# Kernel optimization log

Hardware: AMD Instinct MI355X
Metric: run time of the kernel (lower is better)

## Reference

```python
import jax, jax.numpy as jnp
import numpy as np

TOP_K = 8
SCALE = 2.5  # moe_router_scaling_factor
EPS = 1e-20


def setup_inputs() -> dict:
    key = jax.random.key(0)
    k1, k2 = jax.random.split(key)
    B, S, H, E = 4, 4096, 4096, 64
    hidden_states = jax.random.normal(k1, (B, S, H), dtype=jnp.float32)
    gate_weight = jax.random.normal(k2, (E, H), dtype=jnp.float32) * 0.02
    router_bias = jnp.zeros((E,), dtype=jnp.float32)
    return {"hidden_states": hidden_states, "gate_weight": gate_weight, "router_bias": router_bias}


def reference(hidden_states, gate_weight, router_bias):
    B, S, H = hidden_states.shape
    x = hidden_states.reshape(-1, H).astype(jnp.float32)  # [T, H]
    # need_fp32_gate: fp32 matmul against gate weight transpose -> [T, E]
    logits = jnp.einsum('th,eh->te', x, gate_weight.astype(jnp.float32))
    gate_prob = jax.nn.sigmoid(logits)
    biased = gate_prob + router_bias[None, :]
    # topk on bias-shifted probs; weights gathered from UNbiased probs
    _, indices = jax.lax.top_k(biased, TOP_K)                       # [T, K]
    topk_prob = jnp.take_along_axis(gate_prob, indices, axis=1)     # [T, K]
    weights = topk_prob / (jnp.sum(topk_prob, axis=-1, keepdims=True) + EPS)
    weights = weights * SCALE
    return weights, indices
```

## Files before the change

kernel.cpp:

```cpp
#include <hip/hip_runtime.h>
#include <cmath>


typedef float f32x4 __attribute__((ext_vector_type(4)));
typedef short s16x8 __attribute__((ext_vector_type(8)));
typedef unsigned int u32;
typedef u32 u32x4 __attribute__((ext_vector_type(4)));

#define E_DIM 64
#define KC 32
#define CH_BYTES 12288
#define NPART 4
#define HI_OFF (2u << 20)

union V16 { u32x4 u; s16x8 s; };

__device__ __forceinline__ unsigned short f2bf(float f) {
  unsigned u = __float_as_uint(f);
  u += 0x7fffu + ((u >> 16) & 1u);
  return (unsigned short)(u >> 16);
}
__device__ __forceinline__ float bf2f(unsigned short s) {
  return __uint_as_float(((unsigned)s) << 16);
}

__global__ __launch_bounds__(256) void split_w(
    const float* __restrict__ w, unsigned char* __restrict__ w3, int Hdim)
{
  const int kpr = Hdim >> 4;
  const int g = blockIdx.x * 256 + threadIdx.x;
  const int e = g / kpr;
  const int k0 = (g - e * kpr) * 16;
  if (e >= E_DIM) return;

  const float* src = w + (size_t)e * Hdim + k0;
  float f[16];
#pragma unroll
  for (int i = 0; i < 4; ++i) {
    float4 v = *(const float4*)(src + i * 4);
    f[i*4+0] = v.x; f[i*4+1] = v.y; f[i*4+2] = v.z; f[i*4+3] = v.w;
  }
  unsigned short hs[16], ms[16], ls[16];
#pragma unroll
  for (int i = 0; i < 16; ++i) {
    unsigned short h = f2bf(f[i]);
    float r1 = f[i] - bf2f(h);
    unsigned short m = f2bf(r1);
    float r2 = r1 - bf2f(m);
    hs[i] = h; ms[i] = m; ls[i] = f2bf(r2);
  }
  const int c  = k0 >> 5;
  const int n  = e >> 4;
  const int la = (e & 15) + (((k0 & 31) >> 3) << 4);
  unsigned char* base = w3 + (size_t)c * CH_BYTES + n * 1024;

#define STORE_SPLIT(arr, s)                                              \
  do {                                                                   \
    s16x8 pa, pb;                                                        \
    _Pragma("unroll")                                                    \
    for (int j = 0; j < 8; ++j) { pa[j] = (short)arr[j]; pb[j] = (short)arr[8+j]; } \
    *(s16x8*)(base + (s)*4096 + la * 16)        = pa;                    \
    *(s16x8*)(base + (s)*4096 + (la + 16) * 16) = pb;                    \
  } while (0)

  STORE_SPLIT(hs, 0);
  STORE_SPLIT(ms, 1);
  STORE_SPLIT(ls, 2);
#undef STORE_SPLIT
}

__global__ __launch_bounds__(256, 4) void router_mfma(
    const float* __restrict__ x, const unsigned char* __restrict__ w3,
    const float* __restrict__ bias, float* __restrict__ outw,
    float* __restrict__ outi, float2* __restrict__ pp,
    int T, int Hdim)
{
  __shared__ __align__(16) unsigned char lds[3 * CH_BYTES];

  const int tid  = threadIdx.x;
  const int wid  = tid >> 6;
  const int lane = tid & 63;
  const int lc   = lane & 15;
  const int lq   = lane >> 4;
  const int by   = blockIdx.y;
  const int nch  = Hdim / KC / gridDim.y;
  const int t0   = blockIdx.x * 64;

  const float* xp = x + (size_t)(t0 + wid * 16 + lc) * Hdim
                      + (size_t)by * nch * KC + lq * 8;
  const unsigned char* w3p = w3 + (size_t)by * nch * CH_BYTES;

  f32x4 acc[4], sum_[4], comp[4];
#pragma unroll
  for (int n = 0; n < 4; ++n) {
    acc[n] = (f32x4){0,0,0,0};
    sum_[n] = (f32x4){0,0,0,0};
    comp[n] = (f32x4){0,0,0,0};
  }

#define SB()     __builtin_amdgcn_sched_barrier(0)
#define WAITV5() asm volatile("s_waitcnt vmcnt(5)" ::: "memory")
#define WAITV0() asm volatile("s_waitcnt vmcnt(0)" ::: "memory")
#define BAR()    __builtin_amdgcn_s_barrier()

#define STAGE(c, so)                                                         \
  do {                                                                       \
    const unsigned char* gs = w3p + (size_t)(c) * CH_BYTES + tid * 16;       \
    unsigned char* ld_ = &lds[0] + (so) + tid * 16;                          \
    _Pragma("unroll")                                                        \
    for (int i = 0; i < 3; ++i)                                              \
      __builtin_amdgcn_global_load_lds(                                      \
          (const __attribute__((address_space(1))) unsigned int*)(gs + i*4096), \
          (__attribute__((address_space(3))) unsigned int*)(ld_ + i*4096),   \
          16, 0, 0);                                                         \
  } while (0)

#define LOADX(c, X)                                                          \
  do {                                                                       \
    X[0] = *(const float4*)(xp + (size_t)(c) * KC);                          \
    X[1] = *(const float4*)(xp + (size_t)(c) * KC + 4);                      \
  } while (0)

#define SPLIT_PAIR(f0, f1, i, AHU, AMU, ALU)                                 \
  do {                                                                       \
    u32 u0_ = __float_as_uint(f0), u1_ = __float_as_uint(f1);                \
    u32 v0_ = u0_ + 0x8000u, v1_ = u1_ + 0x8000u;                            \
    AHU[i] = __builtin_amdgcn_perm(v1_, v0_, 0x07060302u);                   \
    float r0_ = (f0) - __uint_as_float(v0_ & 0xffff0000u);                   \
    float r1_ = (f1) - __uint_as_float(v1_ & 0xffff0000u);                   \
    u32 w0_ = __float_as_uint(r0_) + 0x8000u;                                \
    u32 w1_ = __float_as_uint(r1_) + 0x8000u;                                \
    AMU[i] = __builtin_amdgcn_perm(w1_, w0_, 0x07060302u);                   \
    float s0_ = r0_ - __uint_as_float(w0_ & 0xffff0000u);                    \
    float s1_ = r1_ - __uint_as_float(w1_ & 0xffff0000u);                    \
    u32 y0_ = __float_as_uint(s0_) + 0x8000u;                                \
    u32 y1_ = __float_as_uint(s1_) + 0x8000u;                                \
    ALU[i] = __builtin_amdgcn_perm(y1_, y0_, 0x07060302u);                   \
  } while (0)

#define CONVERT(X)                                                           \
  do {                                                                       \
    V16 ah_, am_, al_;                                                       \
    SPLIT_PAIR(X[0].x, X[0].y, 0, ah_.u, am_.u, al_.u);                      \
    SPLIT_PAIR(X[0].z, X[0].w, 1, ah_.u, am_.u, al_.u);                      \
    SPLIT_PAIR(X[1].x, X[1].y, 2, ah_.u, am_.u, al_.u);                      \
    SPLIT_PAIR(X[1].z, X[1].w, 3, ah_.u, am_.u, al_.u);                      \
    Aah = ah_.s; Aam = am_.s; Aal = al_.s;                                   \
  } while (0)

#define MFMA_ALL(ro)                                                         \
  do {                                                                       \
    const unsigned char* B_ = &lds[0] + (ro) + lane * 16;                    \
    __builtin_amdgcn_s_setprio(1);                                           \
    _Pragma("unroll")                                                        \
    for (int g = 0; g < 2; ++g) {                                            \
      s16x8 bh0 = *(const s16x8*)(B_ + 0*4096 + (2*g)*1024);                 \
      s16x8 bh1 = *(const s16x8*)(B_ + 0*4096 + (2*g+1)*1024);               \
      s16x8 bm0 = *(const s16x8*)(B_ + 1*4096 + (2*g)*1024);                 \
      s16x8 bm1 = *(const s16x8*)(B_ + 1*4096 + (2*g+1)*1024);               \
      s16x8 bl0 = *(const s16x8*)(B_ + 2*4096 + (2*g)*1024);                 \
      s16x8 bl1 = *(const s16x8*)(B_ + 2*4096 + (2*g+1)*1024);               \
      acc[2*g]   = __builtin_amdgcn_mfma_f32_16x16x32_bf16(Aah, bh0, acc[2*g],   0,0,0); \
      acc[2*g+1] = __builtin_amdgcn_mfma_f32_16x16x32_bf16(Aah, bh1, acc[2*g+1], 0,0,0); \
      acc[2*g]   = __builtin_amdgcn_mfma_f32_16x16x32_bf16(Aah, bm0, acc[2*g],   0,0,0); \
      acc[2*g+1] = __builtin_amdgcn_mfma_f32_16x16x32_bf16(Aah, bm1, acc[2*g+1], 0,0,0); \
      acc[2*g]   = __builtin_amdgcn_mfma_f32_16x16x32_bf16(Aam, bh0, acc[2*g],   0,0,0); \
      acc[2*g+1] = __builtin_amdgcn_mfma_f32_16x16x32_bf16(Aam, bh1, acc[2*g+1], 0,0,0); \
      acc[2*g]   = __builtin_amdgcn_mfma_f32_16x16x32_bf16(Aah, bl0, acc[2*g],   0,0,0); \
      acc[2*g+1] = __builtin_amdgcn_mfma_f32_16x16x32_bf16(Aah, bl1, acc[2*g+1], 0,0,0); \
      acc[2*g]   = __builtin_amdgcn_mfma_f32_16x16x32_bf16(Aam, bm0, acc[2*g],   0,0,0); \
      acc[2*g+1] = __builtin_amdgcn_mfma_f32_16x16x32_bf16(Aam, bm1, acc[2*g+1], 0,0,0); \
      acc[2*g]   = __builtin_amdgcn_mfma_f32_16x16x32_bf16(Aal, bh0, acc[2*g],   0,0,0); \
      acc[2*g+1] = __builtin_amdgcn_mfma_f32_16x16x32_bf16(Aal, bh1, acc[2*g+1], 0,0,0); \
    }                                                                        \
    __builtin_amdgcn_s_setprio(0);                                           \
  } while (0)

#define FOLD()                                                               \
  do {                                                                       \
    _Pragma("unroll")                                                        \
    for (int n = 0; n < 4; ++n)                                              \
      _Pragma("unroll")                                                      \
      for (int r = 0; r < 4; ++r) {                                          \
        float a_ = acc[n][r];                                                \
        float s_ = sum_[n][r];                                               \
        float t_ = s_ + a_;                                                  \
        float z_ = t_ - s_;                                                  \
        comp[n][r] += (s_ - (t_ - z_)) + (a_ - z_);                          \
        sum_[n][r] = t_;                                                     \
        acc[n][r] = 0.f;                                                     \
      }                                                                      \
  } while (0)

#define ITER(c, ro, so, XBUF)                                                \
  do {                                                                       \
    STAGE((c) + 2, so);                                                      \
    CONVERT(XBUF);                                                           \
    LOADX((c) + 2, XBUF);                                                    \
    SB();                                                                    \
    MFMA_ALL(ro);                                                            \
    WAITV5();                                                                \
    BAR();                                                                   \
  } while (0)

  float4 XA[2], XB[2];
  s16x8 Aah, Aam, Aal;

  int ro0 = 0, ro1 = CH_BYTES, ro2 = 2 * CH_BYTES;

  STAGE(0, ro0);
  STAGE(1, ro1);
  LOADX(0, XA);
  LOADX(1, XB);

#pragma unroll 1
  for (int c = 0; c < nch - 4; c += 4) {
    ITER(c + 0, ro0, ro2, XA);
    ITER(c + 1, ro1, ro0, XB);
    ITER(c + 2, ro2, ro1, XA);
    ITER(c + 3, ro0, ro2, XB);
    FOLD();
    int t_ = ro0; ro0 = ro1; ro1 = ro2; ro2 = t_;
  }
  ITER(nch - 4, ro0, ro2, XA);
  ITER(nch - 3, ro1, ro0, XB);
  {
    CONVERT(XA);
    SB();
    MFMA_ALL(ro2);
    WAITV0();
    BAR();
    CONVERT(XB);
    SB();
    MFMA_ALL(ro0);
    FOLD();
  }

  if (gridDim.y != 1) {
#pragma unroll
    for (int n = 0; n < 4; ++n)
#pragma unroll
      for (int r = 0; r < 4; ++r) {
        const int tok = t0 + wid * 16 + lq * 4 + r;
        const size_t o = ((size_t)tok * NPART + by) * E_DIM + n * 16 + lc;
        pp[o] = make_float2(sum_[n][r], comp[n][r]);
      }
    return;
  }

  float bias_v[4];
#pragma unroll
  for (int n = 0; n < 4; ++n) bias_v[n] = bias[n * 16 + lc];

  float pr[4][4], bi[4][4];
#pragma unroll
  for (int n = 0; n < 4; ++n)
#pragma unroll
    for (int r = 0; r < 4; ++r) {
      float logit = sum_[n][r] + comp[n][r];
      float p = 1.0f / (1.0f + expf(-logit));
      pr[n][r] = p;
      bi[n][r] = p + bias_v[n];
    }
#pragma unroll
  for (int r = 0; r < 4; ++r) {
    float v0 = bi[0][r], v1 = bi[1][r], v2 = bi[2][r], v3 = bi[3][r];
    float p0 = pr[0][r], p1 = pr[1][r], p2 = pr[2][r], p3 = pr[3][r];
    float sum = 0.f, selp = 0.f;
    int seli = 0;
#pragma unroll
    for (int k = 0; k < 8; ++k) {
      float bv = v0; int bn = 0; float bp = p0;
      if (v1 > bv) { bv = v1; bn = 1; bp = p1; }
      if (v2 > bv) { bv = v2; bn = 2; bp = p2; }
      if (v3 > bv) { bv = v3; bn = 3; bp = p3; }
      int be = bn * 16 + lc;
#pragma unroll
      for (int off = 8; off >= 1; off >>= 1) {
        float ov = __shfl_xor(bv, off);
        float op = __shfl_xor(bp, off);
        int   oe = __shfl_xor(be, off);
        if (ov > bv || (ov == bv && oe < be)) { bv = ov; bp = op; be = oe; }
      }
      sum += bp;
      if (lc == k) { selp = bp; seli = be; }
      if (lc == (be & 15)) {
        int gsel = be >> 4;
        if      (gsel == 0) v0 = -1e30f;
        else if (gsel == 1) v1 = -1e30f;
        else if (gsel == 2) v2 = -1e30f;
        else                v3 = -1e30f;
      }
    }
    if (lc < 8) {
      const int tok = t0 + wid * 16 + lq * 4 + r;
      outw[(size_t)tok * 8 + lc] = selp * 2.5f / (sum + 1e-20f);
      outi[(size_t)tok * 8 + lc] = (float)seli;
    }
  }
}

__global__ __launch_bounds__(256) void router_topk(
    const float2* __restrict__ pp, const float* __restrict__ bias,
    float* __restrict__ outw, float* __restrict__ outi, int T)
{
  const int lane = threadIdx.x & 63;
  const int t = blockIdx.x * 4 + (threadIdx.x >> 6);
  if (t >= T) return;

  float s = 0.f, c = 0.f, losum = 0.f;
#pragma unroll
  for (int p = 0; p < NPART; ++p) {
    const float2 v = pp[((size_t)t * NPART + p) * E_DIM + lane];
    float a = v.x;
    float tt = s + a;
    float z = tt - s;
    c += (s - (tt - z)) + (a - z);
    s = tt;
    losum += v.y;
  }
  const float logit = s + (c + losum);

  const float prob = 1.0f / (1.0f + expf(-logit));
  float v = prob + bias[lane];

  float sum = 0.f, selw = 0.f;
  int seli = 0;
#pragma unroll
  for (int k = 0; k < 8; ++k) {
    float rv = v;
    int   ri = lane;
#pragma unroll
    for (int off = 32; off > 0; off >>= 1) {
      float ov = __shfl_xor(rv, off);
      int   oi = __shfl_xor(ri, off);
      if (ov > rv || (ov == rv && oi < ri)) { rv = ov; ri = oi; }
    }
    float pwin = __shfl(prob, ri);
    sum += pwin;
    if (lane == k)  { selw = pwin; seli = ri; }
    if (lane == ri) v = -INFINITY;
  }

  if (lane < 8) {
    float scale = 2.5f / (sum + 1e-20f);
    outw[(size_t)t * 8 + lane] = selw * scale;
    outi[(size_t)t * 8 + lane] = (float)seli;
  }
}

extern "C" void kernel_launch(void* const* d_in, const int* in_sizes, int n_in,
                              void* d_out, int out_size, void* d_ws, size_t ws_size,
                              hipStream_t stream) {
  const float* x    = (const float*)d_in[0];
  const float* w    = (const float*)d_in[1];
  const float* bias = (const float*)d_in[2];

  const int E    = in_sizes[2];
  const int Hdim = in_sizes[1] / E;
  const int T    = in_sizes[0] / Hdim;

  unsigned char* ws = (unsigned char*)d_ws;
  unsigned char* w3 = ws;
  float2* pp = (float2*)(ws + HI_OFF);

  const size_t need = (size_t)HI_OFF + (size_t)NPART * T * E_DIM * sizeof(float2);
  const int nparts = (ws_size >= need) ? NPART : 1;

  const int nElemGroups = E * Hdim / 16;
  split_w<<<(nElemGroups + 255) / 256, 256, 0, stream>>>(w, w3, Hdim);

  float* outw = (float*)d_out;
  float* outi = outw + (size_t)T * 8;

  dim3 gridG(T / 64, nparts);
  router_mfma<<<gridG, 256, 0, stream>>>(x, w3, bias, outw, outi, pp, T, Hdim);

  if (nparts != 1) {
    router_topk<<<(T + 3) / 4, 256, 0, stream>>>(pp, bias, outw, outi, T);
  }
}
```

Measured before the change: 109.9 us.

## Double-buffer weight LDS, split K eight ways, pack partials as single float

Shrinks the weight LDS ring from three stages to two, prefetching one chunk ahead instead of two, and raises the occupancy hint from 4 to 5 blocks per CU. The K dimension is split into 8 partitions instead of 4, doubling the grid. Each partition now writes one float (sum plus compensation) rather than a float2, and the top-k kernel drops its separate low-part sum. The MFMA loop is restructured to iterate per expert tile. The aim is more parallelism and occupancy, at the cost of a shallower prefetch that may expose load latency.

After: 138.9 us. +26.4%, slower.

```diff
diff --git a/kernel.cpp b/kernel.cpp
--- a/kernel.cpp
+++ b/kernel.cpp
@@ -10,7 +10,7 @@
 #define E_DIM 64
 #define KC 32
 #define CH_BYTES 12288
-#define NPART 4
+#define NPART 8
 #define HI_OFF (2u << 20)
 
 union V16 { u32x4 u; s16x8 s; };
@@ -69,13 +69,13 @@
 #undef STORE_SPLIT
 }
 
-__global__ __launch_bounds__(256, 4) void router_mfma(
+__global__ __launch_bounds__(256, 5) void router_mfma(
     const float* __restrict__ x, const unsigned char* __restrict__ w3,
     const float* __restrict__ bias, float* __restrict__ outw,
-    float* __restrict__ outi, float2* __restrict__ pp,
+    float* __restrict__ outi, float* __restrict__ pp,
     int T, int Hdim)
 {
-  __shared__ __align__(16) unsigned char lds[3 * CH_BYTES];
+  __shared__ __align__(16) unsigned char lds[2][CH_BYTES];
 
   const int tid  = threadIdx.x;
   const int wid  = tid >> 6;
@@ -99,14 +99,14 @@
   }
 
 #define SB()     __builtin_amdgcn_sched_barrier(0)
-#define WAITV5() asm volatile("s_waitcnt vmcnt(5)" ::: "memory")
+#define WAITV2() asm volatile("s_waitcnt vmcnt(2)" ::: "memory")
 #define WAITV0() asm volatile("s_waitcnt vmcnt(0)" ::: "memory")
 #define BAR()    __builtin_amdgcn_s_barrier()
 
-#define STAGE(c, so)                                                         \
+#define STAGE(c, b)                                                          \
   do {                                                                       \
     const unsigned char* gs = w3p + (size_t)(c) * CH_BYTES + tid * 16;       \
-    unsigned char* ld_ = &lds[0] + (so) + tid * 16;                          \
+    unsigned char* ld_ = &lds[b][0] + tid * 16;                              \
     _Pragma("unroll")                                                        \
     for (int i = 0; i < 3; ++i)                                              \
       __builtin_amdgcn_global_load_lds(                                      \
@@ -148,30 +148,21 @@
     Aah = ah_.s; Aam = am_.s; Aal = al_.s;                                   \
   } while (0)
 
-#define MFMA_ALL(ro)                                                         \
-  do {                                                                       \
-    const unsigned char* B_ = &lds[0] + (ro) + lane * 16;                    \
+#define MFMA_ALL(b)                                                          \
+  do {                                                                       \
+    const unsigned char* B_ = &lds[b][0] + lane * 16;                        \
     __builtin_amdgcn_s_setprio(1);                                           \
     _Pragma("unroll")                                                        \
-    for (int g = 0; g < 2; ++g) {                                            \
-      s16x8 bh0 = *(const s16x8*)(B_ + 0*4096 + (2*g)*1024);                 \
-      s16x8 bh1 = *(const s16x8*)(B_ + 0*4096 + (2*g+1)*1024);               \
-      s16x8 bm0 = *(const s16x8*)(B_ + 1*4096 + (2*g)*1024);                 \
-      s16x8 bm1 = *(const s16x8*)(B_ + 1*4096 + (2*g+1)*1024);               \
-      s16x8 bl0 = *(const s16x8*)(B_ + 2*4096 + (2*g)*1024);                 \
-      s16x8 bl1 = *(const s16x8*)(B_ + 2*4096 + (2*g+1)*1024);               \
-      acc[2*g]   = __builtin_amdgcn_mfma_f32_16x16x32_bf16(Aah, bh0, acc[2*g],   0,0,0); \
-      acc[2*g+1] = __builtin_amdgcn_mfma_f32_16x16x32_bf16(Aah, bh1, acc[2*g+1], 0,0,0); \
-      acc[2*g]   = __builtin_amdgcn_mfma_f32_16x16x32_bf16(Aah, bm0, acc[2*g],   0,0,0); \
-      acc[2*g+1] = __builtin_amdgcn_mfma_f32_16x16x32_bf16(Aah, bm1, acc[2*g+1], 0,0,0); \
-      acc[2*g]   = __builtin_amdgcn_mfma_f32_16x16x32_bf16(Aam, bh0, acc[2*g],   0,0,0); \
-      acc[2*g+1] = __builtin_amdgcn_mfma_f32_16x16x32_bf16(Aam, bh1, acc[2*g+1], 0,0,0); \
-      acc[2*g]   = __builtin_amdgcn_mfma_f32_16x16x32_bf16(Aah, bl0, acc[2*g],   0,0,0); \
-      acc[2*g+1] = __builtin_amdgcn_mfma_f32_16x16x32_bf16(Aah, bl1, acc[2*g+1], 0,0,0); \
-      acc[2*g]   = __builtin_amdgcn_mfma_f32_16x16x32_bf16(Aam, bm0, acc[2*g],   0,0,0); \
-      acc[2*g+1] = __builtin_amdgcn_mfma_f32_16x16x32_bf16(Aam, bm1, acc[2*g+1], 0,0,0); \
-      acc[2*g]   = __builtin_amdgcn_mfma_f32_16x16x32_bf16(Aal, bh0, acc[2*g],   0,0,0); \
-      acc[2*g+1] = __builtin_amdgcn_mfma_f32_16x16x32_bf16(Aal, bh1, acc[2*g+1], 0,0,0); \
+    for (int n = 0; n < 4; ++n) {                                            \
+      s16x8 bh = *(const s16x8*)(B_ + 0*4096 + n*1024);                      \
+      s16x8 bm = *(const s16x8*)(B_ + 1*4096 + n*1024);                      \
+      s16x8 bl = *(const s16x8*)(B_ + 2*4096 + n*1024);                      \
+      acc[n] = __builtin_amdgcn_mfma_f32_16x16x32_bf16(Aah, bh, acc[n], 0,0,0); \
+      acc[n] = __builtin_amdgcn_mfma_f32_16x16x32_bf16(Aah, bm, acc[n], 0,0,0); \
+      acc[n] = __builtin_amdgcn_mfma_f32_16x16x32_bf16(Aam, bh, acc[n], 0,0,0); \
+      acc[n] = __builtin_amdgcn_mfma_f32_16x16x32_bf16(Aah, bl, acc[n], 0,0,0); \
+      acc[n] = __builtin_amdgcn_mfma_f32_16x16x32_bf16(Aam, bm, acc[n], 0,0,0); \
+      acc[n] = __builtin_amdgcn_mfma_f32_16x16x32_bf16(Aal, bh, acc[n], 0,0,0); \
     }                                                                        \
     __builtin_amdgcn_s_setprio(0);                                           \
   } while (0)
@@ -192,47 +183,49 @@
       }                                                                      \
   } while (0)
 
-#define ITER(c, ro, so, XBUF)                                                \
-  do {                                                                       \
-    STAGE((c) + 2, so);                                                      \
+#define ITER(c, XBUF)                                                        \
+  do {                                                                       \
     CONVERT(XBUF);                                                           \
+    STAGE((c) + 1, ((c) + 1) & 1);                                           \
     LOADX((c) + 2, XBUF);                                                    \
     SB();                                                                    \
-    MFMA_ALL(ro);                                                            \
-    WAITV5();                                                                \
+    MFMA_ALL((c) & 1);                                                       \
+    WAITV2();                                                                \
     BAR();                                                                   \
+    SB();                                                                    \
   } while (0)
 
   float4 XA[2], XB[2];
   s16x8 Aah, Aam, Aal;
 
-  int ro0 = 0, ro1 = CH_BYTES, ro2 = 2 * CH_BYTES;
-
-  STAGE(0, ro0);
-  STAGE(1, ro1);
+  STAGE(0, 0);
   LOADX(0, XA);
   LOADX(1, XB);
+  asm volatile("s_waitcnt vmcnt(4)" ::: "memory");
+  BAR();
+  SB();
 
 #pragma unroll 1
   for (int c = 0; c < nch - 4; c += 4) {
-    ITER(c + 0, ro0, ro2, XA);
-    ITER(c + 1, ro1, ro0, XB);
-    ITER(c + 2, ro2, ro1, XA);
-    ITER(c + 3, ro0, ro2, XB);
+    ITER(c + 0, XA);
+    ITER(c + 1, XB);
+    ITER(c + 2, XA);
+    ITER(c + 3, XB);
     FOLD();
-    int t_ = ro0; ro0 = ro1; ro1 = ro2; ro2 = t_;
-  }
-  ITER(nch - 4, ro0, ro2, XA);
-  ITER(nch - 3, ro1, ro0, XB);
+  }
+  ITER(nch - 4, XA);
+  ITER(nch - 3, XB);
   {
     CONVERT(XA);
+    STAGE(nch - 1, 1);
     SB();
-    MFMA_ALL(ro2);
+    MFMA_ALL(0);
     WAITV0();
     BAR();
+    SB();
     CONVERT(XB);
     SB();
-    MFMA_ALL(ro0);
+    MFMA_ALL(1);
     FOLD();
   }
 
@@ -243,7 +236,7 @@
       for (int r = 0; r < 4; ++r) {
         const int tok = t0 + wid * 16 + lq * 4 + r;
         const size_t o = ((size_t)tok * NPART + by) * E_DIM + n * 16 + lc;
-        pp[o] = make_float2(sum_[n][r], comp[n][r]);
+        pp[o] = sum_[n][r] + comp[n][r];
       }
     return;
   }
@@ -301,25 +294,23 @@
 }
 
 __global__ __launch_bounds__(256) void router_topk(
-    const float2* __restrict__ pp, const float* __restrict__ bias,
+    const float* __restrict__ pp, const float* __restrict__ bias,
     float* __restrict__ outw, float* __restrict__ outi, int T)
 {
   const int lane = threadIdx.x & 63;
   const int t = blockIdx.x * 4 + (threadIdx.x >> 6);
   if (t >= T) return;
 
-  float s = 0.f, c = 0.f, losum = 0.f;
+  float s = 0.f, c = 0.f;
 #pragma unroll
   for (int p = 0; p < NPART; ++p) {
-    const float2 v = pp[((size_t)t * NPART + p) * E_DIM + lane];
-    float a = v.x;
+    float a = pp[((size_t)t * NPART + p) * E_DIM + lane];
     float tt = s + a;
     float z = tt - s;
     c += (s - (tt - z)) + (a - z);
     s = tt;
-    losum += v.y;
-  }
-  const float logit = s + (c + losum);
+  }
+  const float logit = s + c;
 
   const float prob = 1.0f / (1.0f + expf(-logit));
   float v = prob + bias[lane];
@@ -362,9 +353,9 @@
 
   unsigned char* ws = (unsigned char*)d_ws;
   unsigned char* w3 = ws;
-  float2* pp = (float2*)(ws + HI_OFF);
-
-  const size_t need = (size_t)HI_OFF + (size_t)NPART * T * E_DIM * sizeof(float2);
+  float* pp = (float*)(ws + HI_OFF);
+
+  const size_t need = (size_t)HI_OFF + (size_t)NPART * T * E_DIM * sizeof(float);
   const int nparts = (ws_size >= need) ? NPART : 1;
 
   const int nElemGroups = E * Hdim / 16;
```
